# Optimization experiments

Measured on AMD Instinct MI355X. Metric: run time of the kernel, lower is better.

## Reference

```python
import jax, jax.numpy as jnp
import numpy as np
from itertools import combinations

A = 4          # anchor_points
K = 16         # neighbor_num
INTRA = A * (A - 1) // 2   # 6
CH = INTRA * 2 + A * A     # 28 = generator channels
B, N, S = 1, 8192, 4096
CIN, COUT = 64, 128


def cdist(x):
    # pairwise euclidean distances [B,N,N], zero-safe sqrt (zero grad at d=0)
    sq = jnp.sum(x * x, -1)
    d2 = sq[:, :, None] + sq[:, None, :] - 2.0 * jnp.einsum('bnc,bmc->bnm', x, x)
    d2 = jnp.maximum(d2, 0.0)
    m = d2 > 0
    return jnp.where(m, jnp.sqrt(jnp.where(m, d2, 1.0)), 0.0)


def index_points(points, idx):
    # points [B,N,...], idx [B,*] -> [B,*,...]
    return jax.vmap(lambda p, i: p[i])(points, idx)


def index_points_dists(dists, i1, i2):
    # dists [B,N,N]; result[b,...] = dists[b, i1[b,...], i2[b,...]]
    i1, i2 = jnp.broadcast_arrays(i1, i2)
    return jax.vmap(lambda d, a, b: d[a, b])(dists, i1, i2)


def generator(xyz):
    # RotationInvariantDistFea.forward(xyz, concat_raw_relative_fea=True)
    D = cdist(xyz)
    neg_nd, ni = jax.lax.top_k(-D, K)   # K >= A; smallest-K, sorted ascending
    nd = -neg_nd
    ai = ni[:, :, :A]
    # intra-anchor dists: dists to anchors 1..A-1 plus pairwise dists among them
    subs = [index_points_dists(D, ai[:, :, pi], ai[:, :, pj])[:, :, None]
            for pi, pj in combinations(range(1, A), 2)]
    intra = jnp.concatenate([nd[:, :, 1:A]] + subs, axis=2)  # [B,P,6]
    # inter-anchor dists: center anchors x neighbor anchors -> [B,P,K,A*A]
    nai = index_points(ai, ni)                                # [B,P,K,A]
    inter = index_points_dists(D, ai[:, :, None, :, None],
                               nai[:, :, :, None, :]).reshape(D.shape[0], D.shape[1], K, A * A)
    center = jnp.broadcast_to(intra[:, :, None, :], (intra.shape[0], intra.shape[1], K, INTRA))
    rf = jnp.concatenate([center, index_points(intra, ni), inter], axis=3)  # [B,P,K,28]
    return rf, ni, D


def mlp(x, W, b, g, be, act):
    # Linear + BatchNorm1d (training mode: stats over batch*points) + optional leaky_relu(0.2)
    y = x @ W + b
    mu = jnp.mean(y, (0, 1))
    var = jnp.var(y, (0, 1))
    y = (y - mu) * jax.lax.rsqrt(var + 1e-5) * g + be
    return jax.nn.leaky_relu(y, 0.2) if act else y


def forward(xyz, feature, sample_indexes, Ww, bw, gw, betaw, Wb, bb, gb, betab, Wo, bo, go, betao):
    rf_before, ni_before, D_before = generator(xyz)
    intra_before = rf_before[:, :, 0, :INTRA]
    xyz_s = index_points(xyz, sample_indexes)
    feat = index_points(feature, sample_indexes)
    intra_before = index_points(intra_before, sample_indexes)
    rf_after, ni_after, _ = generator(xyz_s)
    intra_after = rf_after[:, :, 0, :INTRA]
    a_before = index_points(ni_before[:, :, :A], sample_indexes)                  # [B,S,A]
    a_after = jax.vmap(lambda s, a: s[a])(sample_indexes, ni_after[:, :, :A])     # map to global idx
    inter = index_points_dists(D_before, a_before[:, :, :, None],
                               a_after[:, :, None, :]).reshape(B, S, A * A)
    adf = jnp.concatenate([intra_before, intra_after, inter], axis=2)             # [B,S,28]
    w = mlp(adf, Ww, bw, gw, betaw, False)
    bia = mlp(adf, Wb, bb, gb, betab, False)
    feat = jax.nn.leaky_relu(feat * w + bia, 0.2)
    feat = jnp.concatenate([feat, adf], axis=2)                                   # [B,S,92]
    feat = mlp(feat, Wo, bo, go, betao, True)                                     # [B,S,128]
    return xyz_s, feat, rf_after, ni_after


def setup_inputs():
    key = jax.random.key(0)
    ks = jax.random.split(key, 8)
    xyz = jax.random.normal(ks[0], (B, N, 3), jnp.float32)
    feature = jax.random.normal(ks[1], (B, N, CIN), jnp.float32)
    sample_indexes = jnp.stack([jax.random.permutation(jax.random.fold_in(ks[2], i), N)[:S]
                                for i in range(B)]).astype(jnp.int32)

    def lin(k, cin, cout):
        k1, k2 = jax.random.split(k)
        W = jax.random.normal(k1, (cin, cout), jnp.float32) / np.float32(np.sqrt(cin))
        b = jax.random.normal(k2, (cout,), jnp.float32) * 0.01
        return W, b, jnp.ones((cout,), jnp.float32), jnp.zeros((cout,), jnp.float32)

    Ww, bw, gw, betaw = lin(ks[5], CH, CIN)
    Wb, bb, gb, betab = lin(ks[6], CH, CIN)
    Wo, bo, go, betao = lin(ks[7], CH + CIN, COUT)
    return dict(xyz=xyz, feature=feature, sample_indexes=sample_indexes,
                Ww=Ww, bw=bw, gw=gw, betaw=betaw,
                Wb=Wb, bb=bb, gb=gb, betab=betab,
                Wo=Wo, bo=bo, go=go, betao=betao)


def reference(xyz, feature, sample_indexes, Ww, bw, gw, betaw, Wb, bb, gb, betab, Wo, bo, go, betao):
    return forward(xyz, feature, sample_indexes, Ww, bw, gw, betaw, Wb, bb, gb, betab, Wo, bo, go, betao)
```

## Files before the change

### kernel.cpp

```cpp
#include <hip/hip_runtime.h>
#include <hip/hip_bf16.h>
#include <math.h>

#define N_PTS 8192
#define S_PTS 4096
typedef unsigned long long u64;
typedef unsigned u32;

__device__ __forceinline__ float pair_dist_d(const float4 a, const float4 b) {
    double ax = a.x, ay = a.y, az = a.z;
    double bx = b.x, by = b.y, bz = b.z;
    double dx = ax - bx, dy = ay - by, dz = az - bz;
    double d2 = dx * dx + dy * dy + dz * dz;
    return d2 > 0.0 ? (float)sqrt(d2) : 0.0f;
}

__device__ __forceinline__ float d2_f32_gram(const float4 a, const float4 b) {
    float dot = __fadd_rn(__fadd_rn(__fmul_rn(a.x, b.x), __fmul_rn(a.y, b.y)),
                          __fmul_rn(a.z, b.z));
    float d2 = __fsub_rn(__fadd_rn(a.w, b.w), __fmul_rn(2.0f, dot));
    return fmaxf(d2, 0.0f);
}

__global__ __launch_bounds__(256) void stage_kernel(
        const float* __restrict__ xyz, const int* __restrict__ sidx,
        float4* __restrict__ cb, float4* __restrict__ ca,
        float* __restrict__ out_xyz_s) {
    int i = blockIdx.x * blockDim.x + threadIdx.x;
    if (i < N_PTS) {
        float x = xyz[i * 3 + 0], y = xyz[i * 3 + 1], z = xyz[i * 3 + 2];
        float sq = __fadd_rn(__fadd_rn(__fmul_rn(x, x), __fmul_rn(y, y)),
                             __fmul_rn(z, z));
        cb[i] = make_float4(x, y, z, sq);
    }
    if (i < S_PTS) {
        int si = sidx[i];
        float x = xyz[si * 3 + 0], y = xyz[si * 3 + 1], z = xyz[si * 3 + 2];
        float sq = __fadd_rn(__fadd_rn(__fmul_rn(x, x), __fmul_rn(y, y)),
                             __fmul_rn(z, z));
        ca[i] = make_float4(x, y, z, sq);
        out_xyz_s[i * 3 + 0] = x;
        out_xyz_s[i * 3 + 1] = y;
        out_xyz_s[i * 3 + 2] = z;
    }
}


template <int KOUT, int ITERS>
__device__ u64 knn_full_ladder(const float4 q, const float4* __restrict__ cand,
                               int lane) {
    u32 Lk[KOUT], Li[KOUT];
#pragma unroll
    for (int j = 0; j < KOUT; ++j) { Lk[j] = 0xFFFFFFFFu; Li[j] = 0xFFFFFFFFu; }
    int c = lane;
    for (int tt = 0; tt < ITERS; ++tt, c += 64) {
        float d2 = d2_f32_gram(q, cand[c]);
        float Df = d2 > 0.0f ? __fsqrt_rn(d2) : 0.0f;
        u32 kb = __float_as_uint(Df);
        if (kb < Lk[KOUT - 1]) {
#pragma unroll
            for (int j = KOUT - 1; j >= 1; --j) {
                bool up = kb < Lk[j - 1], ins = kb < Lk[j];
                Lk[j] = up ? Lk[j - 1] : (ins ? kb : Lk[j]);
                Li[j] = up ? Li[j - 1] : (ins ? (u32)c : Li[j]);
            }
            bool i0 = kb < Lk[0];
            Lk[0] = i0 ? kb : Lk[0];
            Li[0] = i0 ? (u32)c : Li[0];
        }
    }
    u64 Lu[KOUT];
#pragma unroll
    for (int j = 0; j < KOUT; ++j) Lu[j] = ((u64)Lk[j] << 32) | (u64)Li[j];
    u64 res = ~0ull;
#pragma unroll
    for (int r = 0; r < KOUT; ++r) {
        u64 m = Lu[0];
#pragma unroll
        for (int off = 32; off >= 1; off >>= 1) {
            u64 o = __shfl_xor(m, off, 64);
            m = (o < m) ? o : m;
        }
        if (lane == r) res = m;
        if (Lu[0] == m) {
#pragma unroll
            for (int j = 0; j < KOUT - 1; ++j) Lu[j] = Lu[j + 1];
            Lu[KOUT - 1] = ~0ull;
        }
    }
    return res;
}

template <int K, int NC>
__device__ u64 final_select(const float4 qq, const float4* __restrict__ cand,
                            const u64* bufq, u32 cnt, int lane) {
    if (cnt <= 64u) {
        u64 v = (lane < (int)cnt) ? bufq[lane] : ~0ull;
#pragma unroll
        for (int k = 2; k <= 64; k <<= 1) {
#pragma unroll
            for (int j2 = k >> 1; j2 >= 1; j2 >>= 1) {
                u64 o = __shfl_xor(v, j2, 64);
                bool keepMin = (((lane & j2) == 0) == ((lane & k) == 0));
                bool less = o < v;
                v = keepMin ? (less ? o : v) : (less ? v : o);
            }
        }
        return v;
    } else if (cnt <= 256u) {
        u64 L0 = ~0ull, L1 = ~0ull, L2 = ~0ull, L3 = ~0ull;
        for (u32 mm = lane; mm < cnt; mm += 64) {
            u64 kk = bufq[mm];
            if (kk < L3) {
                if (kk < L1) {
                    L3 = L2; L2 = L1;
                    if (kk < L0) { L1 = L0; L0 = kk; } else L1 = kk;
                } else {
                    if (kk < L2) { L3 = L2; L2 = kk; } else L3 = kk;
                }
            }
        }
        u64 res = ~0ull;
#pragma unroll
        for (int r = 0; r < K; ++r) {
            u64 mr = L0;
#pragma unroll
            for (int off = 32; off >= 1; off >>= 1) {
                u64 o = __shfl_xor(mr, off, 64);
                mr = (o < mr) ? o : mr;
            }
            if (lane == r) res = mr;
            if (L0 == mr) { L0 = L1; L1 = L2; L2 = L3; L3 = ~0ull; }
        }
        return res;
    }
    return knn_full_ladder<K, NC / 64>(qq, cand, lane);
}

template <int J, int K, int NC, int Q>
__device__ __forceinline__ u64 knn_selectq(
        const float4* qs, const float4* __restrict__ cand, int t,
        u32* mins, u64* buf, u32* shm) {
    int lane = t & 63, wid = t >> 6;
    u32 d2b[Q][J];
    u32 m[Q];
#pragma unroll
    for (int qi = 0; qi < Q; ++qi) m[qi] = 0xFFFFFFFFu;
#pragma unroll
    for (int j = 0; j < J; ++j) {
        float4 c = cand[t + 256 * j];
#pragma unroll
        for (int qi = 0; qi < Q; ++qi) {
            u32 b = __float_as_uint(d2_f32_gram(qs[qi], c));
            d2b[qi][j] = b;
            m[qi] = b < m[qi] ? b : m[qi];
        }
    }
#pragma unroll
    for (int qi = 0; qi < Q; ++qi) mins[qi * 256 + t] = m[qi];
    __syncthreads();
    if (wid < Q) {
        const u32* mq = mins + wid * 256;
        u32 v = mq[lane];
        u32 v2 = mq[lane + 64];  v = v2 < v ? v2 : v;
        v2 = mq[lane + 128];     v = v2 < v ? v2 : v;
        v2 = mq[lane + 192];     v = v2 < v ? v2 : v;
#pragma unroll
        for (int k = 2; k <= 64; k <<= 1) {
#pragma unroll
            for (int j2 = k >> 1; j2 >= 1; j2 >>= 1) {
                u32 o = __shfl_xor(v, j2, 64);
                bool keepMin = (((lane & j2) == 0) == ((lane & k) == 0));
                bool less = o < v;
                v = keepMin ? (less ? o : v) : (less ? v : o);
            }
        }
        if (lane == K - 1) shm[wid] = v;
    }
    __syncthreads();
    u32 tau[Q], c[Q], x[Q];
#pragma unroll
    for (int qi = 0; qi < Q; ++qi) {
        tau[qi] = shm[qi];
        u32 cc = 0;
#pragma unroll
        for (int j = 0; j < J; ++j) cc += (d2b[qi][j] <= tau[qi]) ? 1u : 0u;
        c[qi] = cc;
        u32 xx = cc;
#pragma unroll
        for (int off = 1; off < 64; off <<= 1) {
            u32 y = __shfl_up(xx, off, 64);
            if (lane >= off) xx += y;
        }
        x[qi] = xx;
        if (lane == 63) shm[Q + qi * 4 + wid] = xx;
    }
    __syncthreads();
    u32 cnt[Q];
#pragma unroll
    for (int qi = 0; qi < Q; ++qi) {
        u32 base = x[qi] - c[qi];
        for (int w = 0; w < wid; ++w) base += shm[Q + qi * 4 + w];
        cnt[qi] = shm[Q + qi * 4 + 0] + shm[Q + qi * 4 + 1] +
                  shm[Q + qi * 4 + 2] + shm[Q + qi * 4 + 3];
        if (cnt[qi] <= 256u) {
            u32 off = base;
#pragma unroll
            for (int j = 0; j < J; ++j) {
                if (d2b[qi][j] <= tau[qi]) {
                    float d2 = __uint_as_float(d2b[qi][j]);
                    float D = d2 > 0.0f ? __fsqrt_rn(d2) : 0.0f;
                    buf[qi * 256 + off++] = ((u64)__float_as_uint(D) << 32) |
                                            (u64)(u32)(t + 256 * j);
                }
            }
        }
    }
    __syncthreads();
    u64 res = ~0ull;
#pragma unroll
    for (int qi = 0; qi < Q; ++qi)
        if (wid == qi)
            res = final_select<K, NC>(qs[qi], cand, buf + qi * 256, cnt[qi], lane);
    return res;
}

__global__ __launch_bounds__(256, 4) void knn_kernel(
        const float4* __restrict__ cb, const float4* __restrict__ ca,
        const int* __restrict__ sidx,
        int* __restrict__ a_before, float* __restrict__ intra_before,
        int* __restrict__ ni_i, float* __restrict__ intra_after,
        float* __restrict__ out_ni) {
    __shared__ u32 mins[4 * 256];
    __shared__ u64 buf[4 * 256];
    __shared__ u32 shm[24];
    int t = threadIdx.x, lane = t & 63, wid = t >> 6;
    int bid = blockIdx.x;
    if (bid < S_PTS / 4) {
        int s0 = bid * 4;
        float4 qs[4];
#pragma unroll
        for (int qi = 0; qi < 4; ++qi) qs[qi] = ca[s0 + qi];
        u64 res = knn_selectq<16, 16, 4096, 4>(qs, ca, t, mins, buf, shm);
        if (wid < 4) {
            int s = s0 + wid;
            float4 qq = ca[s];
            int idx = (int)(res & 0xffffffffull);
            if (lane < 16) {
                ni_i[s * 16 + lane] = idx;
                out_ni[s * 16 + lane] = (float)idx;
            }
            if (lane >= 1 && lane < 4)
                intra_after[s * 6 + (lane - 1)] = pair_dist_d(qq, ca[idx]);
            int i1 = __shfl(idx, 1, 64);
            int i2 = __shfl(idx, 2, 64);
            int i3 = __shfl(idx, 3, 64);
            if (lane < 3) {
                int pa = (lane == 2) ? i2 : i1;
                int pb = (lane == 0) ? i2 : i3;
                intra_after[s * 6 + 3 + lane] = pair_dist_d(ca[pa], ca[pb]);
            }
        }
    } else {
        int s0 = (bid - S_PTS / 4) * 2;
        float4 qs[2];
        qs[0] = cb[sidx[s0]];
        qs[1] = cb[sidx[s0 + 1]];
        u64 res = knn_selectq<32, 4, 8192, 2>(qs, cb, t, mins, buf, shm);
        if (wid < 2) {
            int s = s0 + wid;
            float4 qq = cb[sidx[s]];
            int idx = (int)(res & 0xffffffffull);
            if (lane < 4) a_before[s * 4 + lane] = idx;
            if (lane >= 1 && lane < 4)
                intra_before[s * 6 + (lane - 1)] = pair_dist_d(qq, cb[idx]);
            int i1 = __shfl(idx, 1, 64);
            int i2 = __shfl(idx, 2, 64);
            int i3 = __shfl(idx, 3, 64);
            if (lane < 3) {
                int pa = (lane == 2) ? i2 : i1;
                int pb = (lane == 0) ? i2 : i3;
                intra_before[s * 6 + 3 + lane] = pair_dist_d(cb[pa], cb[pb]);
            }
        }
    }
}

__global__ __launch_bounds__(256) void assemble_kernel(
        const float4* __restrict__ ca, const float4* __restrict__ cb,
        const int* __restrict__ ni_i, const float* __restrict__ intra_after,
        const int* __restrict__ a_before, const float* __restrict__ intra_before,
        const int* __restrict__ sidx,
        float* __restrict__ out_rf, float* __restrict__ adf) {
    __shared__ int s_ni[4][16];
    __shared__ float s_rf[4][16 * 28];
    __shared__ float s_ia[4][8];
    int t = threadIdx.x, wid = t >> 6, lane = t & 63;
    int s = blockIdx.x * 4 + wid;
    if (lane < 16) s_ni[wid][lane] = ni_i[s * 16 + lane];
    if (lane < 6) s_ia[wid][lane] = intra_after[s * 6 + lane];
    __syncthreads();

    int k = lane >> 2, qq = lane & 3;
    int nai_q = ni_i[s_ni[wid][k] * 16 + qq];
    float4 pq = ca[nai_q];
#pragma unroll
    for (int p = 0; p < 4; ++p) {
        float4 pp = ca[s_ni[wid][p]];
        s_rf[wid][k * 28 + 12 + p * 4 + qq] = pair_dist_d(pp, pq);
    }
    for (int idx = lane; idx < 16 * 12; idx += 64) {
        int kk = idx / 12, c = idx % 12;
        float v = (c < 6) ? s_ia[wid][c] : intra_after[s_ni[wid][kk] * 6 + (c - 6)];
        s_rf[wid][kk * 28 + c] = v;
    }
    if (lane < 16) {
        int p = lane >> 2, q2 = lane & 3;
        int ib = a_before[s * 4 + p];
        int ia = sidx[s_ni[wid][q2]];
        adf[s * 28 + 12 + lane] = pair_dist_d(cb[ib], cb[ia]);
    } else if (lane >= 32 && lane < 38) {
        adf[s * 28 + (lane - 32)] = intra_before[s * 6 + (lane - 32)];
    } else if (lane >= 40 && lane < 46) {
        adf[s * 28 + 6 + (lane - 40)] = s_ia[wid][lane - 40];
    }
    __syncthreads();
    const int base = s * 16 * 28;
    for (int idx = lane; idx < 16 * 28; idx += 64) out_rf[base + idx] = s_rf[wid][idx];
}

__global__ __launch_bounds__(256) void mlp1_kernel(
        const float* __restrict__ adf,
        const float* __restrict__ Ww, const float* __restrict__ bw,
        const float* __restrict__ Wb, const float* __restrict__ bb,
        float* __restrict__ y_wb) {
    __shared__ float sW[28 * 128];
    __shared__ float sb[128];
    __shared__ float sA[32 * 28];
    int t = threadIdx.x;
    for (int i = t; i < 28 * 128; i += 256) {
        int k = i >> 7, c = i & 127;
        sW[i] = (c < 64) ? Ww[k * 64 + c] : Wb[k * 64 + (c - 64)];
    }
    if (t < 128) sb[t] = (t < 64) ? bw[t] : bb[t - 64];
    int s0 = blockIdx.x * 32;
    for (int i = t; i < 32 * 28; i += 256) sA[i] = adf[s0 * 28 + i];
    __syncthreads();
    int sl = t >> 3, grp = t & 7;
    int s = s0 + sl;
    float acc[16];
#pragma unroll
    for (int k = 0; k < 16; ++k) acc[k] = sb[grp * 16 + k];
    for (int k2 = 0; k2 < 28; ++k2) {
        float a = sA[sl * 28 + k2];
#pragma unroll
        for (int k = 0; k < 16; ++k)
            acc[k] = fmaf(a, sW[k2 * 128 + grp * 16 + k], acc[k]);
    }
#pragma unroll
    for (int k = 0; k < 16; ++k) y_wb[(grp * 16 + k) * 4096 + s] = acc[k];
}

__global__ __launch_bounds__(256) void stats_kernel(
        const float* __restrict__ y,
        const float* __restrict__ g0, const float* __restrict__ be0,
        const float* __restrict__ g1, const float* __restrict__ be1, int csplit,
        float* __restrict__ scale, float* __restrict__ shift) {
    int c = blockIdx.x;
    const float* p = y + c * 4096;
    float s1 = 0.0f, s2 = 0.0f;
    for (int i = threadIdx.x; i < 4096; i += 256) {
        float v = p[i];
        s1 += v;
        s2 = fmaf(v, v, s2);
    }
    __shared__ float l1[256], l2[256];
    l1[threadIdx.x] = s1;
    l2[threadIdx.x] = s2;
    __syncthreads();
    for (int off = 128; off; off >>= 1) {
        if (threadIdx.x < off) {
            l1[threadIdx.x] += l1[threadIdx.x + off];
            l2[threadIdx.x] += l2[threadIdx.x + off];
        }
        __syncthreads();
    }
    if (threadIdx.x == 0) {
        float mean = l1[0] * (1.0f / 4096.0f);
        float var = l2[0] * (1.0f / 4096.0f) - mean * mean;
        float g = (c < csplit) ? g0[c] : g1[c - csplit];
        float be = (c < csplit) ? be0[c] : be1[c - csplit];
        float sc = g / sqrtf(var + 1e-5f);
        scale[c] = sc;
        shift[c] = be - mean * sc;
    }
}

__global__ __launch_bounds__(256) void mlp2_kernel(
        const float* __restrict__ y_wb,
        const float* __restrict__ scale1, const float* __restrict__ shift1,
        const float* __restrict__ feature, const int* __restrict__ sidx,
        const float* __restrict__ adf,
        const float* __restrict__ Wo, const float* __restrict__ bo,
        float* __restrict__ y_o) {
    __shared__ float sW[92 * 128];
    __shared__ float t2[16 * 129];
    __shared__ float scat[16 * 92];
    int t = threadIdx.x;
    int s0 = blockIdx.x * 16;
    for (int i = t; i < 92 * 128; i += 256) sW[i] = Wo[i];
    for (int i = t; i < 16 * 128; i += 256) {
        int row = i & 15, c = i >> 4;
        t2[row * 129 + c] = fmaf(y_wb[c * 4096 + s0 + row], scale1[c], shift1[c]);
    }
    __syncthreads();
    for (int rr = 0; rr < 16; rr += 4) {
        int r = rr + (t >> 6);
        int c = t & 63;
        int si = sidx[s0 + r];
        float f = feature[si * 64 + c];
        float v = fmaf(f, t2[r * 129 + c], t2[r * 129 + 64 + c]);
        scat[r * 92 + c] = v >= 0.0f ? v : 0.2f * v;
    }
    for (int i = t; i < 16 * 28; i += 256) {
        int row = i / 28, k = i % 28;
        scat[row * 92 + 64 + k] = adf[(s0 + row) * 28 + k];
    }
    __syncthreads();
    int r = t >> 4, cg = t & 15;
    float acc[8];
#pragma unroll
    for (int j = 0; j < 8; ++j) acc[j] = bo[cg * 8 + j];
    for (int c = 0; c < 92; ++c) {
        float a = scat[r * 92 + c];
#pragma unroll
        for (int j = 0; j < 8; ++j)
            acc[j] = fmaf(a, sW[c * 128 + cg * 8 + j], acc[j]);
    }
    int s = s0 + r;
#pragma unroll
    for (int j = 0; j < 8; ++j) y_o[(cg * 8 + j) * 4096 + s] = acc[j];
}

__global__ __launch_bounds__(256) void final_kernel(
        const float* __restrict__ y_o,
        const float* __restrict__ scale, const float* __restrict__ shift,
        float* __restrict__ out_feat) {
    int tid = blockIdx.x * 256 + threadIdx.x;
    int j = tid >> 12;
    int s = tid & 4095;
    float v = fmaf(y_o[tid], scale[j], shift[j]);
    v = v >= 0.0f ? v : 0.2f * v;
    out_feat[s * 128 + j] = v;
}

extern "C" void kernel_launch(void* const* d_in, const int* in_sizes, int n_in,
                              void* d_out, int out_size, void* d_ws, size_t ws_size,
                              hipStream_t stream) {
    const float* xyz = (const float*)d_in[0];
    const float* feature = (const float*)d_in[1];
    const int* sidx = (const int*)d_in[2];
    const float* Ww = (const float*)d_in[3];
    const float* bw = (const float*)d_in[4];
    const float* gw = (const float*)d_in[5];
    const float* betaw = (const float*)d_in[6];
    const float* Wb = (const float*)d_in[7];
    const float* bb = (const float*)d_in[8];
    const float* gb = (const float*)d_in[9];
    const float* betab = (const float*)d_in[10];
    const float* Wo = (const float*)d_in[11];
    const float* bo = (const float*)d_in[12];
    const float* go = (const float*)d_in[13];
    const float* betao = (const float*)d_in[14];

    float* out = (float*)d_out;
    float* out_xyz = out;
    float* out_feat = out + 12288;
    float* out_rf = out + 12288 + 524288;
    float* out_ni = out + 12288 + 524288 + 1835008;

    float* ws = (float*)d_ws;
    float4* cb = (float4*)ws;
    float4* ca = (float4*)(ws + 32768);
    int* a_before = (int*)(ws + 49152);
    float* intra_before = ws + 65536;
    int* ni_i = (int*)(ws + 90112);
    float* intra_after = ws + 155648;
    float* adf = ws + 180224;
    float* y_wb = ws + 294912;
    float* y_o = ws + 819200;
    float* scale1 = ws + 1343488;
    float* shift1 = ws + 1343616;
    float* scale_o = ws + 1343744;
    float* shift_o = ws + 1343872;

    stage_kernel<<<32, 256, 0, stream>>>(xyz, sidx, cb, ca, out_xyz);
    knn_kernel<<<S_PTS / 4 + S_PTS / 2, 256, 0, stream>>>(
        cb, ca, sidx, a_before, intra_before, ni_i, intra_after, out_ni);
    assemble_kernel<<<1024, 256, 0, stream>>>(ca, cb, ni_i, intra_after, a_before,
                                              intra_before, sidx, out_rf, adf);
    mlp1_kernel<<<128, 256, 0, stream>>>(adf, Ww, bw, Wb, bb, y_wb);
    stats_kernel<<<128, 256, 0, stream>>>(y_wb, gw, betaw, gb, betab, 64, scale1, shift1);
    mlp2_kernel<<<256, 256, 0, stream>>>(y_wb, scale1, shift1, feature, sidx, adf, Wo, bo, y_o);
    stats_kernel<<<128, 256, 0, stream>>>(y_o, go, betao, go, betao, 128, scale_o, shift_o);
    final_kernel<<<2048, 256, 0, stream>>>(y_o, scale_o, shift_o, out_feat);
}
```

Baseline: 166.6 us.

## Use fp32 Gram distances, reuse kNN distances, fuse final stats and activation

```diff
diff --git a/kernel.cpp b/kernel.cpp
--- a/kernel.cpp
+++ b/kernel.cpp
@@ -6,20 +6,17 @@
 #define S_PTS 4096
 typedef unsigned long long u64;
 typedef unsigned u32;
-
-__device__ __forceinline__ float pair_dist_d(const float4 a, const float4 b) {
-    double ax = a.x, ay = a.y, az = a.z;
-    double bx = b.x, by = b.y, bz = b.z;
-    double dx = ax - bx, dy = ay - by, dz = az - bz;
-    double d2 = dx * dx + dy * dy + dz * dz;
-    return d2 > 0.0 ? (float)sqrt(d2) : 0.0f;
-}
 
 __device__ __forceinline__ float d2_f32_gram(const float4 a, const float4 b) {
     float dot = __fadd_rn(__fadd_rn(__fmul_rn(a.x, b.x), __fmul_rn(a.y, b.y)),
                           __fmul_rn(a.z, b.z));
     float d2 = __fsub_rn(__fadd_rn(a.w, b.w), __fmul_rn(2.0f, dot));
     return fmaxf(d2, 0.0f);
+}
+
+__device__ __forceinline__ float pair_dist_f(const float4 a, const float4 b) {
+    float d2 = d2_f32_gram(a, b);
+    return d2 > 0.0f ? __fsqrt_rn(d2) : 0.0f;
 }
 
 __global__ __launch_bounds__(256) void stage_kernel(
@@ -244,21 +241,21 @@
         u64 res = knn_selectq<16, 16, 4096, 4>(qs, ca, t, mins, buf, shm);
         if (wid < 4) {
             int s = s0 + wid;
-            float4 qq = ca[s];
             int idx = (int)(res & 0xffffffffull);
             if (lane < 16) {
                 ni_i[s * 16 + lane] = idx;
                 out_ni[s * 16 + lane] = (float)idx;
             }
             if (lane >= 1 && lane < 4)
-                intra_after[s * 6 + (lane - 1)] = pair_dist_d(qq, ca[idx]);
+                intra_after[s * 6 + (lane - 1)] =
+                    __uint_as_float((u32)(res >> 32));
             int i1 = __shfl(idx, 1, 64);
             int i2 = __shfl(idx, 2, 64);
             int i3 = __shfl(idx, 3, 64);
             if (lane < 3) {
                 int pa = (lane == 2) ? i2 : i1;
                 int pb = (lane == 0) ? i2 : i3;
-                intra_after[s * 6 + 3 + lane] = pair_dist_d(ca[pa], ca[pb]);
+                intra_after[s * 6 + 3 + lane] = pair_dist_f(ca[pa], ca[pb]);
             }
         }
     } else {
@@ -269,18 +266,18 @@
         u64 res = knn_selectq<32, 4, 8192, 2>(qs, cb, t, mins, buf, shm);
         if (wid < 2) {
             int s = s0 + wid;
-            float4 qq = cb[sidx[s]];
             int idx = (int)(res & 0xffffffffull);
             if (lane < 4) a_before[s * 4 + lane] = idx;
             if (lane >= 1 && lane < 4)
-                intra_before[s * 6 + (lane - 1)] = pair_dist_d(qq, cb[idx]);
+                intra_before[s * 6 + (lane - 1)] =
+                    __uint_as_float((u32)(res >> 32));
             int i1 = __shfl(idx, 1, 64);
             int i2 = __shfl(idx, 2, 64);
             int i3 = __shfl(idx, 3, 64);
             if (lane < 3) {
                 int pa = (lane == 2) ? i2 : i1;
                 int pb = (lane == 0) ? i2 : i3;
-                intra_before[s * 6 + 3 + lane] = pair_dist_d(cb[pa], cb[pb]);
+                intra_before[s * 6 + 3 + lane] = pair_dist_f(cb[pa], cb[pb]);
             }
         }
     }
@@ -307,7 +304,7 @@
 #pragma unroll
     for (int p = 0; p < 4; ++p) {
         float4 pp = ca[s_ni[wid][p]];
-        s_rf[wid][k * 28 + 12 + p * 4 + qq] = pair_dist_d(pp, pq);
+        s_rf[wid][k * 28 + 12 + p * 4 + qq] = pair_dist_f(pp, pq);
     }
     for (int idx = lane; idx < 16 * 12; idx += 64) {
         int kk = idx / 12, c = idx % 12;
@@ -318,7 +315,7 @@
         int p = lane >> 2, q2 = lane & 3;
         int ib = a_before[s * 4 + p];
         int ia = sidx[s_ni[wid][q2]];
-        adf[s * 28 + 12 + lane] = pair_dist_d(cb[ib], cb[ia]);
+        adf[s * 28 + 12 + lane] = pair_dist_f(cb[ib], cb[ia]);
     } else if (lane >= 32 && lane < 38) {
         adf[s * 28 + (lane - 32)] = intra_before[s * 6 + (lane - 32)];
     } else if (lane >= 40 && lane < 46) {
@@ -442,16 +439,44 @@
     for (int j = 0; j < 8; ++j) y_o[(cg * 8 + j) * 4096 + s] = acc[j];
 }
 
-__global__ __launch_bounds__(256) void final_kernel(
+__global__ __launch_bounds__(256) void stats_final_kernel(
         const float* __restrict__ y_o,
-        const float* __restrict__ scale, const float* __restrict__ shift,
+        const float* __restrict__ go, const float* __restrict__ betao,
         float* __restrict__ out_feat) {
-    int tid = blockIdx.x * 256 + threadIdx.x;
-    int j = tid >> 12;
-    int s = tid & 4095;
-    float v = fmaf(y_o[tid], scale[j], shift[j]);
-    v = v >= 0.0f ? v : 0.2f * v;
-    out_feat[s * 128 + j] = v;
+    int c = blockIdx.x;
+    const float* p = y_o + c * 4096;
+    float s1 = 0.0f, s2 = 0.0f;
+    for (int i = threadIdx.x; i < 4096; i += 256) {
+        float v = p[i];
+        s1 += v;
+        s2 = fmaf(v, v, s2);
+    }
+    __shared__ float l1[256], l2[256];
+    __shared__ float s_sc, s_sh;
+    l1[threadIdx.x] = s1;
+    l2[threadIdx.x] = s2;
+    __syncthreads();
+    for (int off = 128; off; off >>= 1) {
+        if (threadIdx.x < off) {
+            l1[threadIdx.x] += l1[threadIdx.x + off];
+            l2[threadIdx.x] += l2[threadIdx.x + off];
+        }
+        __syncthreads();
+    }
+    if (threadIdx.x == 0) {
+        float mean = l1[0] * (1.0f / 4096.0f);
+        float var = l2[0] * (1.0f / 4096.0f) - mean * mean;
+        float sc = go[c] / sqrtf(var + 1e-5f);
+        s_sc = sc;
+        s_sh = betao[c] - mean * sc;
+    }
+    __syncthreads();
+    float sc = s_sc, sh = s_sh;
+    for (int i = threadIdx.x; i < 4096; i += 256) {
+        float v = fmaf(p[i], sc, sh);
+        v = v >= 0.0f ? v : 0.2f * v;
+        out_feat[i * 128 + c] = v;
+    }
 }
 
 extern "C" void kernel_launch(void* const* d_in, const int* in_sizes, int n_in,
@@ -491,8 +516,6 @@
     float* y_o = ws + 819200;
     float* scale1 = ws + 1343488;
     float* shift1 = ws + 1343616;
-    float* scale_o = ws + 1343744;
-    float* shift_o = ws + 1343872;
 
     stage_kernel<<<32, 256, 0, stream>>>(xyz, sidx, cb, ca, out_xyz);
     knn_kernel<<<S_PTS / 4 + S_PTS / 2, 256, 0, stream>>>(
@@ -502,6 +525,5 @@
     mlp1_kernel<<<128, 256, 0, stream>>>(adf, Ww, bw, Wb, bb, y_wb);
     stats_kernel<<<128, 256, 0, stream>>>(y_wb, gw, betaw, gb, betab, 64, scale1, shift1);
     mlp2_kernel<<<256, 256, 0, stream>>>(y_wb, scale1, shift1, feature, sidx, adf, Wo, bo, y_o);
-    stats_kernel<<<128, 256, 0, stream>>>(y_o, go, betao, go, betao, 128, scale_o, shift_o);
-    final_kernel<<<2048, 256, 0, stream>>>(y_o, scale_o, shift_o, out_feat);
-}
+    stats_final_kernel<<<128, 256, 0, stream>>>(y_o, go, betao, out_feat);
+}
```

Measured after the change: 166.4 us. About the same (-0.2%).
